# Performance work log

Hardware: AMD Instinct MI355X
Metric: run time of the kernel (lower is better)

## Reference

```python
import jax, jax.numpy as jnp
import numpy as np
from jax import lax

DIM = 4096
N_HEADS = 32
N_KV_HEADS = 8
HEAD_DIM = DIM // N_HEADS  # 128
N_REP = N_HEADS // N_KV_HEADS  # 4
B, S = 1, 2048
ROPE_THETA = 10000.0
NEG_INF = -1e9


def setup_inputs() -> dict:
    key = jax.random.key(0)
    ks = jax.random.split(key, 6)
    scale = 1.0 / np.sqrt(DIM)
    x = jax.random.normal(ks[0], (B, S, DIM), dtype=jnp.float32)
    wq = jax.random.normal(ks[1], (DIM, DIM), dtype=jnp.float32) * scale
    wk = jax.random.normal(ks[2], (N_KV_HEADS * HEAD_DIM, DIM), dtype=jnp.float32) * scale
    wv = jax.random.normal(ks[3], (N_KV_HEADS * HEAD_DIM, DIM), dtype=jnp.float32) * scale
    wo = jax.random.normal(ks[4], (DIM, DIM), dtype=jnp.float32) * scale
    # Llama rotary frequencies: freqs_cis[t, i] = exp(i * t * theta^(-2i/d))
    inv_freq = 1.0 / (ROPE_THETA ** (np.arange(0, HEAD_DIM, 2, dtype=np.float32) / HEAD_DIM))
    angles = np.outer(np.arange(S, dtype=np.float32), inv_freq)  # [S, HEAD_DIM//2]
    freqs_cos = jnp.asarray(np.cos(angles), dtype=jnp.float32)
    freqs_sin = jnp.asarray(np.sin(angles), dtype=jnp.float32)
    cache_k = jnp.zeros((B, S, N_KV_HEADS, HEAD_DIM), dtype=jnp.float32)
    cache_v = jnp.zeros((B, S, N_KV_HEADS, HEAD_DIM), dtype=jnp.float32)
    # causal mask added to scores (broadcasts over [B, H, S, S])
    mask = jnp.where(np.triu(np.ones((S, S), dtype=bool), k=1), NEG_INF, 0.0).astype(jnp.float32)
    return {"x": x, "wq": wq, "wk": wk, "wv": wv, "wo": wo,
            "freqs_cos": freqs_cos, "freqs_sin": freqs_sin,
            "cache_k": cache_k, "cache_v": cache_v, "mask": mask,
            "start_pos": 0}


def _apply_rotary(t, cos, sin):
    # t: [B, S, H, HEAD_DIM]; cos/sin: [S, HEAD_DIM//2]
    b, s, h, d = t.shape
    tr = t.reshape(b, s, h, d // 2, 2)
    a, bb = tr[..., 0], tr[..., 1]  # real / imag of consecutive pairs
    c = cos[None, :, None, :]
    sn = sin[None, :, None, :]
    out_r = a * c - bb * sn
    out_i = a * sn + bb * c
    return jnp.stack([out_r, out_i], axis=-1).reshape(b, s, h, d)


def reference(x, wq, wk, wv, wo, freqs_cos, freqs_sin, cache_k, cache_v, mask, start_pos):
    bsz, seqlen, _ = x.shape
    xq = jnp.einsum('bsd,od->bso', x, wq).reshape(bsz, seqlen, N_HEADS, HEAD_DIM)
    xk = jnp.einsum('bsd,od->bso', x, wk).reshape(bsz, seqlen, N_KV_HEADS, HEAD_DIM)
    xv = jnp.einsum('bsd,od->bso', x, wv).reshape(bsz, seqlen, N_KV_HEADS, HEAD_DIM)
    xq = _apply_rotary(xq, freqs_cos, freqs_sin)
    xk = _apply_rotary(xk, freqs_cos, freqs_sin)
    # KV-cache append
    cache_k = lax.dynamic_update_slice(cache_k, xk, (0, start_pos, 0, 0))
    cache_v = lax.dynamic_update_slice(cache_v, xv, (0, start_pos, 0, 0))
    kv_len = start_pos + seqlen
    keys = cache_k[:, :kv_len]    # [B, KVLEN, KV, HD]
    values = cache_v[:, :kv_len]
    # GQA: repeat_interleave over kv heads
    keys = jnp.repeat(keys, N_REP, axis=2)      # [B, KVLEN, H, HD]
    values = jnp.repeat(values, N_REP, axis=2)
    q = xq.transpose(0, 2, 1, 3)       # [B, H, S, HD]
    k = keys.transpose(0, 2, 1, 3)     # [B, H, KVLEN, HD]
    v = values.transpose(0, 2, 1, 3)
    scores = jnp.einsum('bhqd,bhkd->bhqk', q, k) / np.sqrt(HEAD_DIM)
    scores = scores + mask[None, None, :, :]
    probs = jax.nn.softmax(scores.astype(jnp.float32), axis=-1).astype(q.dtype)
    out = jnp.einsum('bhqk,bhkd->bhqd', probs, v)
    out = out.transpose(0, 2, 1, 3).reshape(bsz, seqlen, -1)
    return jnp.einsum('bso,do->bsd', out, wo)
```

## Files before the change

kernel.cpp:

```cpp
#include <hip/hip_runtime.h>
#include <hip/hip_bf16.h>

typedef unsigned short u16;
typedef unsigned int u32;
typedef __bf16 bf16x8 __attribute__((ext_vector_type(8)));
typedef float f32x4 __attribute__((ext_vector_type(4)));
typedef u32 u32x4 __attribute__((ext_vector_type(4)));

#define QKV_LD 6144
#define KOFF 4096
#define VOFF 5120
#define HD 128
#define DIM 4096

__device__ __forceinline__ u16 f2bf(float f) {
  union { __hip_bfloat16 h; u16 u; } c;
  c.h = __float2bfloat16(f);
  return c.u;
}
__device__ __forceinline__ float bf2f(u16 u) {
  union { u16 u; __hip_bfloat16 h; } c;
  c.u = u;
  return __bfloat162float(c.h);
}

typedef __attribute__((address_space(1))) const u32 gas_u32;
typedef __attribute__((address_space(3))) u32 las_u32;
__device__ __forceinline__ void async16(const u16* g, u16* l) {
  __builtin_amdgcn_global_load_lds((gas_u32*)g, (las_u32*)l, 16, 0, 0);
}

__device__ __forceinline__ void store_out(u16* p, float v) { *p = f2bf(v); }
__device__ __forceinline__ void store_out(float* p, float v) { *p = v; }

__global__ __launch_bounds__(256) void cvt_kernel(const float* __restrict__ src,
                                                  u16* __restrict__ dst, int n8) {
  int i = blockIdx.x * 256 + threadIdx.x;
  if (i >= n8) return;
  const f32x4* s4 = (const f32x4*)src;
  f32x4 a = s4[2 * i], b = s4[2 * i + 1];
  u32x4 o;
  o[0] = (u32)f2bf(a[0]) | ((u32)f2bf(a[1]) << 16);
  o[1] = (u32)f2bf(a[2]) | ((u32)f2bf(a[3]) << 16);
  o[2] = (u32)f2bf(b[0]) | ((u32)f2bf(b[1]) << 16);
  o[3] = (u32)f2bf(b[2]) | ((u32)f2bf(b[3]) << 16);
  ((u32x4*)dst)[i] = o;
}

template <typename OutT>
__global__ __launch_bounds__(256, 2) void gemm_nt(const u16* __restrict__ A,
                                                  const u16* __restrict__ B,
                                                  OutT* __restrict__ C, int N, int K) {
  __shared__ u16 As[128 * 32];
  __shared__ u16 Bs[128 * 32];
  const int tid = threadIdx.x;
  const int wave = tid >> 6;
  const int lane = tid & 63;
  const int quad = lane >> 4;
  const int l16 = lane & 15;
  const int bm = blockIdx.y;
  const int bn = blockIdx.x;
  const int wm = (wave >> 1) * 64;
  const int wn = (wave & 1) * 64;

  f32x4 acc[4][4];
#pragma unroll
  for (int i = 0; i < 4; ++i)
#pragma unroll
    for (int j = 0; j < 4; ++j) {
      f32x4 z = {0.f, 0.f, 0.f, 0.f};
      acc[i][j] = z;
    }

  const int srow0 = wave * 32 + (lane >> 2);
  const int scol = (((lane & 3) ^ ((lane >> 2) & 3)) * 8);
  u16* ldsA0 = &As[(wave * 2 + 0) * 512];
  u16* ldsA1 = &As[(wave * 2 + 1) * 512];
  u16* ldsB0 = &Bs[(wave * 2 + 0) * 512];
  u16* ldsB1 = &Bs[(wave * 2 + 1) * 512];
  const u16* Ag0 = A + (size_t)(bm * 128 + srow0) * K + scol;
  const u16* Ag1 = A + (size_t)(bm * 128 + srow0 + 16) * K + scol;
  const u16* Bg0 = B + (size_t)(bn * 128 + srow0) * K + scol;
  const u16* Bg1 = B + (size_t)(bn * 128 + srow0 + 16) * K + scol;

  int aoff[4], boff[4];
#pragma unroll
  for (int mi = 0; mi < 4; ++mi)
    aoff[mi] = (wm + mi * 16 + l16) * 32 + ((quad ^ (l16 & 3)) * 8);
#pragma unroll
  for (int ni = 0; ni < 4; ++ni)
    boff[ni] = (wn + ni * 16 + l16) * 32 + ((quad ^ (l16 & 3)) * 8);

  for (int k0 = 0; k0 < K; k0 += 32) {
    __syncthreads();
    async16(Ag0 + k0, ldsA0);
    async16(Ag1 + k0, ldsA1);
    async16(Bg0 + k0, ldsB0);
    async16(Bg1 + k0, ldsB1);
    __syncthreads();
    bf16x8 af[4], bb[4];
#pragma unroll
    for (int mi = 0; mi < 4; ++mi) af[mi] = *(const bf16x8*)&As[aoff[mi]];
#pragma unroll
    for (int ni = 0; ni < 4; ++ni) bb[ni] = *(const bf16x8*)&Bs[boff[ni]];
#pragma unroll
    for (int mi = 0; mi < 4; ++mi)
#pragma unroll
      for (int ni = 0; ni < 4; ++ni)
        acc[mi][ni] = __builtin_amdgcn_mfma_f32_16x16x32_bf16(af[mi], bb[ni], acc[mi][ni], 0, 0, 0);
  }

#pragma unroll
  for (int mi = 0; mi < 4; ++mi) {
    int row = bm * 128 + wm + mi * 16 + quad * 4;
#pragma unroll
    for (int ni = 0; ni < 4; ++ni) {
      int col = bn * 128 + wn + ni * 16 + l16;
#pragma unroll
      for (int r = 0; r < 4; ++r)
        store_out(&C[(size_t)(row + r) * N + col], acc[mi][ni][r]);
    }
  }
}

__global__ __launch_bounds__(256) void rope_kernel(u16* qkv, const float* __restrict__ fcos,
                                                   const float* __restrict__ fsin) {
  int idx = blockIdx.x * 256 + threadIdx.x;
  int row, colbase, fi;
  if (idx < 2048 * 2048) {
    row = idx >> 11;
    int pi = idx & 2047;
    fi = pi & 63;
    colbase = (pi >> 6) * 128 + fi * 2;
  } else {
    int j = idx - 2048 * 2048;
    row = j >> 9;
    int pj = j & 511;
    fi = pj & 63;
    colbase = KOFF + (pj >> 6) * 128 + fi * 2;
  }
  float c = fcos[row * 64 + fi], s = fsin[row * 64 + fi];
  u32* p = (u32*)(qkv + (size_t)row * QKV_LD + colbase);
  u32 v = *p;
  float a = bf2f((u16)(v & 0xffffu));
  float b = bf2f((u16)(v >> 16));
  float xr = a * c - b * s;
  float xi = a * s + b * c;
  *p = (u32)f2bf(xr) | ((u32)f2bf(xi) << 16);
}

__global__ __launch_bounds__(256) void vtrans_kernel(const u16* __restrict__ qkv,
                                                     u16* __restrict__ vt) {
  __shared__ u16 Ls[64 * 72];
  const int tid = threadIdx.x;
  const int st = blockIdx.x, dt = blockIdx.y, kvh = blockIdx.z;
#pragma unroll
  for (int t = 0; t < 2; ++t) {
    int g = t * 256 + tid;
    int s = g >> 3, c = g & 7;
    u32x4 v = *(const u32x4*)(qkv + (size_t)(st * 64 + s) * QKV_LD + VOFF + kvh * HD + dt * 64 + c * 8);
    *(u32x4*)&Ls[s * 72 + c * 8] = v;
  }
  __syncthreads();
#pragma unroll
  for (int t = 0; t < 2; ++t) {
    int g = t * 256 + tid;
    int d = g >> 3, c2 = g & 7;
    u32x4 o;
#pragma unroll
    for (int j = 0; j < 4; ++j) {
      u16 lo = Ls[(c2 * 8 + 2 * j) * 72 + d];
      u16 hi = Ls[(c2 * 8 + 2 * j + 1) * 72 + d];
      o[j] = (u32)lo | ((u32)hi << 16);
    }
    *(u32x4*)(vt + (size_t)(kvh * HD + dt * 64 + d) * 2048 + st * 64 + c2 * 8) = o;
  }
}

__global__ __launch_bounds__(256, 3) void flash_kernel(const u16* __restrict__ qkv,
                                                       const u16* __restrict__ vt,
                                                       u16* __restrict__ attnb) {
  __shared__ u16 Kl[64 * 128];
  __shared__ u16 VtL[128 * 64];
  __shared__ u16 Pl[4][16 * 72];
  const int tid = threadIdx.x;
  const int wave = tid >> 6;
  const int lane = tid & 63;
  const int quad = lane >> 4;
  const int l16 = lane & 15;
  const int qt = 31 - blockIdx.x;
  const int h = blockIdx.y;
  const int kvh = h >> 2;
  const float scale = 0.08838834764831845f;

  bf16x8 qf[4];
  {
    const u16* qp = qkv + (size_t)(qt * 64 + wave * 16 + l16) * QKV_LD + h * HD + quad * 8;
#pragma unroll
    for (int ks = 0; ks < 4; ++ks) qf[ks] = *(const bf16x8*)(qp + ks * 32);
  }

  f32x4 o[8];
#pragma unroll
  for (int i = 0; i < 8; ++i) { f32x4 z = {0.f, 0.f, 0.f, 0.f}; o[i] = z; }
  float mrow[4] = {-1e30f, -1e30f, -1e30f, -1e30f};
  float lrow[4] = {0.f, 0.f, 0.f, 0.f};

  const int krow = (lane >> 4);
  const int kc = 0;
  const int vd_l = (lane >> 3);
  const int vc = (lane & 7) ^ ((lane >> 3) & 7);

  for (int kt = 0; kt <= qt; ++kt) {
    __syncthreads();
#pragma unroll
    for (int t = 0; t < 4; ++t) {
      int i = wave * 4 + t;
      int row = i * 4 + krow;
      int c = (lane & 15) ^ (row & 15);
      async16(qkv + (size_t)(kt * 64 + row) * QKV_LD + KOFF + kvh * HD + c * 8,
              &Kl[i * 512]);
    }
#pragma unroll
    for (int t = 0; t < 4; ++t) {
      int i = wave * 4 + t;
      int d = i * 8 + vd_l;
      async16(vt + (size_t)(kvh * HD + d) * 2048 + kt * 64 + vc * 8,
              &VtL[i * 512]);
    }
    __syncthreads();

    f32x4 s4[4];
#pragma unroll
    for (int nb = 0; nb < 4; ++nb) {
      f32x4 z = {0.f, 0.f, 0.f, 0.f};
      s4[nb] = z;
#pragma unroll
      for (int ks = 0; ks < 4; ++ks) {
        int rr = nb * 16 + l16;
        int cc = ((ks * 4 + quad) ^ l16) * 8;
        bf16x8 kf = *(const bf16x8*)&Kl[rr * 128 + cc];
        s4[nb] = __builtin_amdgcn_mfma_f32_16x16x32_bf16(qf[ks], kf, s4[nb], 0, 0, 0);
      }
    }

    float p[4][4];
    float mx[4] = {-1e30f, -1e30f, -1e30f, -1e30f};
    const bool diag = (kt == qt);
#pragma unroll
    for (int nb = 0; nb < 4; ++nb) {
#pragma unroll
      for (int r = 0; r < 4; ++r) {
        float s = s4[nb][r] * scale;
        if (diag) {
          int col = nb * 16 + l16;
          int rowq = wave * 16 + quad * 4 + r;
          if (col > rowq) s = -1e30f;
        }
        p[nb][r] = s;
        mx[r] = fmaxf(mx[r], s);
      }
    }
#pragma unroll
    for (int r = 0; r < 4; ++r) {
      mx[r] = fmaxf(mx[r], __shfl_xor(mx[r], 1));
      mx[r] = fmaxf(mx[r], __shfl_xor(mx[r], 2));
      mx[r] = fmaxf(mx[r], __shfl_xor(mx[r], 4));
      mx[r] = fmaxf(mx[r], __shfl_xor(mx[r], 8));
    }
    float alpha[4], sum[4];
#pragma unroll
    for (int r = 0; r < 4; ++r) {
      float mnew = fmaxf(mrow[r], mx[r]);
      alpha[r] = __expf(mrow[r] - mnew);
      mrow[r] = mnew;
      float sm = 0.f;
#pragma unroll
      for (int nb = 0; nb < 4; ++nb) {
        float e = __expf(p[nb][r] - mnew);
        p[nb][r] = e;
        sm += e;
      }
      sum[r] = sm;
    }
#pragma unroll
    for (int r = 0; r < 4; ++r) {
      sum[r] += __shfl_xor(sum[r], 1);
      sum[r] += __shfl_xor(sum[r], 2);
      sum[r] += __shfl_xor(sum[r], 4);
      sum[r] += __shfl_xor(sum[r], 8);
      lrow[r] = lrow[r] * alpha[r] + sum[r];
    }
#pragma unroll
    for (int db = 0; db < 8; ++db)
#pragma unroll
      for (int r = 0; r < 4; ++r) o[db][r] *= alpha[r];

#pragma unroll
    for (int nb = 0; nb < 4; ++nb)
#pragma unroll
      for (int r = 0; r < 4; ++r)
        Pl[wave][(quad * 4 + r) * 72 + nb * 16 + l16] = f2bf(p[nb][r]);
    __asm__ __volatile__("s_waitcnt lgkmcnt(0)" ::: "memory");
    bf16x8 pa[2];
#pragma unroll
    for (int ks2 = 0; ks2 < 2; ++ks2)
      pa[ks2] = *(const bf16x8*)&Pl[wave][l16 * 72 + ks2 * 32 + quad * 8];

#pragma unroll
    for (int db = 0; db < 8; ++db) {
      int dd = db * 16 + l16;
#pragma unroll
      for (int ks2 = 0; ks2 < 2; ++ks2) {
        int c = (ks2 * 4 + quad) ^ (dd & 7);
        bf16x8 vb = *(const bf16x8*)&VtL[dd * 64 + c * 8];
        o[db] = __builtin_amdgcn_mfma_f32_16x16x32_bf16(pa[ks2], vb, o[db], 0, 0, 0);
      }
    }
  }

  float inv[4];
#pragma unroll
  for (int r = 0; r < 4; ++r) inv[r] = 1.f / lrow[r];
#pragma unroll
  for (int db = 0; db < 8; ++db) {
#pragma unroll
    for (int r = 0; r < 4; ++r) {
      int row = qt * 64 + wave * 16 + quad * 4 + r;
      int col = h * HD + db * 16 + l16;
      attnb[(size_t)row * DIM + col] = f2bf(o[db][r] * inv[r]);
    }
  }
}

extern "C" void kernel_launch(void* const* d_in, const int* in_sizes, int n_in,
                              void* d_out, int out_size, void* d_ws, size_t ws_size,
                              hipStream_t stream) {
  (void)in_sizes; (void)n_in; (void)out_size; (void)ws_size;
  const float* x    = (const float*)d_in[0];
  const float* wq   = (const float*)d_in[1];
  const float* wk   = (const float*)d_in[2];
  const float* wv   = (const float*)d_in[3];
  const float* wo   = (const float*)d_in[4];
  const float* fcos = (const float*)d_in[5];
  const float* fsin = (const float*)d_in[6];
  float* out = (float*)d_out;

  char* ws = (char*)d_ws;
  u16* xb    = (u16*)(ws);
  u16* wqkvb = (u16*)(ws + (size_t)16777216);
  u16* wob   = (u16*)(ws + (size_t)67108864);
  u16* qkv   = (u16*)(ws + (size_t)100663296);
  u16* attnb = (u16*)(ws + (size_t)125829120);
  u16* vtb   = (u16*)(ws);

  cvt_kernel<<<4096, 256, 0, stream>>>(x, xb, 1048576);
  cvt_kernel<<<8192, 256, 0, stream>>>(wq, wqkvb, 2097152);
  cvt_kernel<<<2048, 256, 0, stream>>>(wk, wqkvb + 16777216, 524288);
  cvt_kernel<<<2048, 256, 0, stream>>>(wv, wqkvb + 20971520, 524288);
  cvt_kernel<<<8192, 256, 0, stream>>>(wo, wob, 2097152);

  gemm_nt<u16><<<dim3(48, 16), 256, 0, stream>>>(xb, wqkvb, qkv, 6144, 4096);
  vtrans_kernel<<<dim3(32, 2, 8), 256, 0, stream>>>(qkv, vtb);
  rope_kernel<<<20480, 256, 0, stream>>>(qkv, fcos, fsin);
  flash_kernel<<<dim3(32, 32), 256, 0, stream>>>(qkv, vtb, attnb);
  gemm_nt<float><<<dim3(32, 16), 256, 0, stream>>>(attnb, wob, out, 4096, 4096);
}
```

Before: 605.0 us.

## Double-buffer K and V tiles in flash attention with next-tile async prefetch

The flash attention kernel now holds two LDS buffers each for the K and V^T tiles. It issues the async loads for tile kt+1 before computing on tile kt, so global-to-LDS traffic overlaps the QK^T, softmax and PV MFMA work, and one of the two barriers per iteration goes away. The cost is doubled K/V LDS, about 73 KB per block, and launch bounds are lowered from 3 to 2 blocks per CU. Less occupancy means less latency hiding across blocks.

```diff
diff --git a/kernel.cpp b/kernel.cpp
--- a/kernel.cpp
+++ b/kernel.cpp
@@ -177,11 +177,11 @@
   }
 }
 
-__global__ __launch_bounds__(256, 3) void flash_kernel(const u16* __restrict__ qkv,
+__global__ __launch_bounds__(256, 2) void flash_kernel(const u16* __restrict__ qkv,
                                                        const u16* __restrict__ vt,
                                                        u16* __restrict__ attnb) {
-  __shared__ u16 Kl[64 * 128];
-  __shared__ u16 VtL[128 * 64];
+  __shared__ u16 Kl[2][64 * 128];
+  __shared__ u16 VtL[2][128 * 64];
   __shared__ u16 Pl[4][16 * 72];
   const int tid = threadIdx.x;
   const int wave = tid >> 6;
@@ -193,6 +193,14 @@
   const int kvh = h >> 2;
   const float scale = 0.08838834764831845f;
 
+  const int krow_l = (lane >> 4);
+  const int kcol_l = (lane & 15);
+  const int vd_l = (lane >> 3);
+  const int vc = (lane & 7) ^ ((lane >> 3) & 7);
+
+  const u16* kbase = qkv + (size_t)KOFF + kvh * HD;
+  const u16* vbase = vt + (size_t)kvh * HD * 2048;
+
   bf16x8 qf[4];
   {
     const u16* qp = qkv + (size_t)(qt * 64 + wave * 16 + l16) * QKV_LD + h * HD + quad * 8;
@@ -206,29 +214,40 @@
   float mrow[4] = {-1e30f, -1e30f, -1e30f, -1e30f};
   float lrow[4] = {0.f, 0.f, 0.f, 0.f};
 
-  const int krow = (lane >> 4);
-  const int kc = 0;
-  const int vd_l = (lane >> 3);
-  const int vc = (lane & 7) ^ ((lane >> 3) & 7);
+#pragma unroll
+  for (int t = 0; t < 4; ++t) {
+    int i = wave * 4 + t;
+    int row = i * 4 + krow_l;
+    int c = kcol_l ^ (row & 15);
+    async16(kbase + (size_t)row * QKV_LD + c * 8, &Kl[0][i * 512]);
+  }
+#pragma unroll
+  for (int t = 0; t < 4; ++t) {
+    int i = wave * 4 + t;
+    int d = i * 8 + vd_l;
+    async16(vbase + (size_t)d * 2048 + vc * 8, &VtL[0][i * 512]);
+  }
 
   for (int kt = 0; kt <= qt; ++kt) {
+    const int cur = kt & 1;
     __syncthreads();
-#pragma unroll
-    for (int t = 0; t < 4; ++t) {
-      int i = wave * 4 + t;
-      int row = i * 4 + krow;
-      int c = (lane & 15) ^ (row & 15);
-      async16(qkv + (size_t)(kt * 64 + row) * QKV_LD + KOFF + kvh * HD + c * 8,
-              &Kl[i * 512]);
-    }
-#pragma unroll
-    for (int t = 0; t < 4; ++t) {
-      int i = wave * 4 + t;
-      int d = i * 8 + vd_l;
-      async16(vt + (size_t)(kvh * HD + d) * 2048 + kt * 64 + vc * 8,
-              &VtL[i * 512]);
-    }
-    __syncthreads();
+    if (kt < qt) {
+      const u16* kb = kbase + (size_t)(kt + 1) * 64 * QKV_LD;
+      const u16* vb = vbase + (kt + 1) * 64;
+#pragma unroll
+      for (int t = 0; t < 4; ++t) {
+        int i = wave * 4 + t;
+        int row = i * 4 + krow_l;
+        int c = kcol_l ^ (row & 15);
+        async16(kb + (size_t)row * QKV_LD + c * 8, &Kl[1 - cur][i * 512]);
+      }
+#pragma unroll
+      for (int t = 0; t < 4; ++t) {
+        int i = wave * 4 + t;
+        int d = i * 8 + vd_l;
+        async16(vb + (size_t)d * 2048 + vc * 8, &VtL[1 - cur][i * 512]);
+      }
+    }
 
     f32x4 s4[4];
 #pragma unroll
@@ -239,7 +258,7 @@
       for (int ks = 0; ks < 4; ++ks) {
         int rr = nb * 16 + l16;
         int cc = ((ks * 4 + quad) ^ l16) * 8;
-        bf16x8 kf = *(const bf16x8*)&Kl[rr * 128 + cc];
+        bf16x8 kf = *(const bf16x8*)&Kl[cur][rr * 128 + cc];
         s4[nb] = __builtin_amdgcn_mfma_f32_16x16x32_bf16(qf[ks], kf, s4[nb], 0, 0, 0);
       }
     }
@@ -313,7 +332,7 @@
 #pragma unroll
       for (int ks2 = 0; ks2 < 2; ++ks2) {
         int c = (ks2 * 4 + quad) ^ (dd & 7);
-        bf16x8 vb = *(const bf16x8*)&VtL[dd * 64 + c * 8];
+        bf16x8 vb = *(const bf16x8*)&VtL[cur][dd * 64 + c * 8];
         o[db] = __builtin_amdgcn_mfma_f32_16x16x32_bf16(pa[ks2], vb, o[db], 0, 0, 0);
       }
     }
```

Result: no change. 597.0 us (-1.3%).
